# Kernel tuning notes

Hardware: AMD Instinct MI355X
Metric: run time of the kernel (lower is better)

Reference implementation:

```python
import jax, jax.numpy as jnp
import numpy as np

N = 1048576   # total points in batch
C_PT = 9      # point feature dim
C_LB = 20     # number of semantic classes (labels as soft/one-hot floats)
V1 = 500000   # unique voxels at scale 1
V8 = 65536    # unique voxels at scale 8


def setup_inputs() -> dict:
    key = jax.random.key(0)
    k1, k2, k3, k4 = jax.random.split(key, 4)
    points = jax.random.normal(k1, (N, C_PT), dtype=jnp.float32)
    coors_inv_s1 = jax.random.randint(k2, (N,), 0, V1, dtype=jnp.int64)
    labels = jax.random.uniform(k3, (N, C_LB), dtype=jnp.float32)
    coors_inv_s8 = jax.random.randint(k4, (N,), 0, V8, dtype=jnp.int64)
    return {"points": points, "coors_inv_s1": coors_inv_s1,
            "labels": labels, "coors_inv_s8": coors_inv_s8}


def _scatter_mean(x, idx, num_segments):
    # torch_scatter.scatter_mean(x, idx, dim=0): per-segment sum / count (count>=1)
    seg_sum = jax.ops.segment_sum(x, idx, num_segments=num_segments)
    ones = jnp.ones((x.shape[0], 1), dtype=x.dtype)
    count = jax.ops.segment_sum(ones, idx, num_segments=num_segments)
    return seg_sum / jnp.maximum(count, jnp.asarray(1, x.dtype))


def reference(points, coors_inv_s1, labels, coors_inv_s8):
    # voxel features: mean of point features per scale-1 voxel  -> [V1, C_PT]
    features = _scatter_mean(points, coors_inv_s1, V1)
    # voxel labels: mean of per-point class vectors per scale-8 voxel -> [V8, C_LB]
    voxel_labels = _scatter_mean(labels, coors_inv_s8, V8)
    # SparseConvTensor construction / dict assignment in the original is
    # bookkeeping; the computed tensors are (features, voxel_labels).
    return features, voxel_labels
```

## Files before the change

### kernel.cpp

```cpp
#include <hip/hip_runtime.h>

#define N_PTS 1048576
#define C_PT 9
#define C_LB 20
#define V1 500000
#define V8 65536

#define NB1 1954
#define NB8 256
#define NBT (NB1 + NB8)
#define KBLOCKS 256
#define PTS_PER_BLOCK (N_PTS / KBLOCKS)
#define CAP 2048

__global__ __launch_bounds__(1024) void count_kernel(const int* __restrict__ inv1,
                                                     const int* __restrict__ inv8,
                                                     unsigned short* __restrict__ mat)
{
    __shared__ int hist[NBT];
    for (int k = threadIdx.x; k < NBT; k += 1024) hist[k] = 0;
    __syncthreads();
    int base_i = blockIdx.x * PTS_PER_BLOCK;
    for (int t = threadIdx.x; t < PTS_PER_BLOCK; t += 1024) {
        int i = base_i + t;
        atomicAdd(&hist[inv1[i] >> 8], 1);
        atomicAdd(&hist[NB1 + (inv8[i] >> 8)], 1);
    }
    __syncthreads();
    unsigned short* row = mat + (size_t)blockIdx.x * NBT;
    for (int k = threadIdx.x; k < NBT; k += 1024) row[k] = (unsigned short)hist[k];
}

__global__ __launch_bounds__(256) void colscan_kernel(unsigned short* __restrict__ mat,
                                                      int* __restrict__ total)
{
    int wave = (int)((blockIdx.x * 256 + threadIdx.x) >> 6);
    int lane = threadIdx.x & 63;
    if (wave >= NBT) return;
    int carry = 0;
    for (int c = 0; c < KBLOCKS; c += 64) {
        int b = c + lane;
        int v = (int)mat[(size_t)b * NBT + wave];
        int s = v;
        #pragma unroll
        for (int d = 1; d < 64; d <<= 1) {
            int u = __shfl_up(s, d, 64);
            if (lane >= d) s += u;
        }
        mat[(size_t)b * NBT + wave] = (unsigned short)(s - v + carry);
        carry += __shfl(s, 63, 64);
    }
    if (lane == 0) total[wave] = carry;
}

__global__ __launch_bounds__(64) void basescan_kernel(const int* __restrict__ total,
                                                      int* __restrict__ base)
{
    int lane = threadIdx.x;
    int carry = 0;
    for (int c = 0; c < NB1; c += 64) {
        int k = c + lane;
        int v = (k < NB1) ? total[k] : 0;
        int s = v;
        #pragma unroll
        for (int d = 1; d < 64; d <<= 1) {
            int u = __shfl_up(s, d, 64);
            if (lane >= d) s += u;
        }
        if (k < NB1) base[k] = s - v + carry;
        carry += __shfl(s, 63, 64);
    }
    carry = 0;
    for (int c = 0; c < NB8; c += 64) {
        int k = c + lane;
        int v = total[NB1 + k];
        int s = v;
        #pragma unroll
        for (int d = 1; d < 64; d <<= 1) {
            int u = __shfl_up(s, d, 64);
            if (lane >= d) s += u;
        }
        base[NB1 + k] = s - v + carry;
        carry += __shfl(s, 63, 64);
    }
}

__global__ __launch_bounds__(1024) void scatter_kernel(const int* __restrict__ inv1,
                                                       const int* __restrict__ inv8,
                                                       const unsigned short* __restrict__ mat,
                                                       const int* __restrict__ base,
                                                       int* __restrict__ sorted1,
                                                       int* __restrict__ sorted8)
{
    __shared__ int off[NBT];
    __shared__ int cnt[NBT];
    const unsigned short* row = mat + (size_t)blockIdx.x * NBT;
    for (int k = threadIdx.x; k < NBT; k += 1024) {
        off[k] = base[k] + (int)row[k];
        cnt[k] = 0;
    }
    __syncthreads();
    int base_i = blockIdx.x * PTS_PER_BLOCK;
    for (int t = threadIdx.x; t < PTS_PER_BLOCK; t += 1024) {
        int i = base_i + t;
        int v1 = inv1[i];
        int k1 = v1 >> 8;
        int r1 = atomicAdd(&cnt[k1], 1);
        sorted1[off[k1] + r1] = i | ((v1 & 255) << 20);
        int v8 = inv8[i];
        int k8 = NB1 + (v8 >> 8);
        int r8 = atomicAdd(&cnt[k8], 1);
        sorted8[off[k8] + r8] = i | ((v8 & 255) << 20);
    }
}

__global__ __launch_bounds__(256) void accum_voxel_kernel(const float* __restrict__ points,
                                                          const float* __restrict__ labels,
                                                          const int* __restrict__ sorted1,
                                                          const int* __restrict__ sorted8,
                                                          const int* __restrict__ base,
                                                          const int* __restrict__ total,
                                                          float* __restrict__ feat_out,
                                                          float* __restrict__ lbl_out)
{
    __shared__ unsigned stage[CAP];
    __shared__ unsigned short perm[CAP];
    __shared__ int hist[256];
    __shared__ int starts[256];
    __shared__ int cursor[256];
    __shared__ int wsum[4];

    const int tid  = threadIdx.x;
    const int lane = tid & 63;
    const int wid  = tid >> 6;

    if (blockIdx.x < NB8) {
        int b = blockIdx.x;
        int start = base[NB1 + b];
        int num   = total[NB1 + b];
        float acc[C_LB];
        #pragma unroll
        for (int c = 0; c < C_LB; ++c) acc[c] = 0.0f;
        int mycnt = 0;

        for (int cbase = 0; cbase < num; cbase += CAP) {
            int csize = min(CAP, num - cbase);
            __syncthreads();
            for (int t = tid; t < csize; t += 256)
                stage[t] = (unsigned)sorted8[start + cbase + t];
            hist[tid] = 0;
            __syncthreads();
            for (int t = tid; t < csize; t += 256)
                atomicAdd(&hist[stage[t] >> 20], 1);
            __syncthreads();
            int x = hist[tid];
            int s = x;
            #pragma unroll
            for (int d = 1; d < 64; d <<= 1) {
                int u = __shfl_up(s, d, 64);
                if (lane >= d) s += u;
            }
            if (lane == 63) wsum[wid] = s;
            __syncthreads();
            int off = 0;
            #pragma unroll
            for (int w = 0; w < 4; ++w) if (w < wid) off += wsum[w];
            starts[tid] = off + s - x;
            cursor[tid] = 0;
            __syncthreads();
            for (int t = tid; t < csize; t += 256) {
                int bin = (int)(stage[t] >> 20);
                int r = atomicAdd(&cursor[bin], 1);
                perm[starts[bin] + r] = (unsigned short)t;
            }
            __syncthreads();
            int n  = hist[tid];
            int s0 = starts[tid];
            for (int j = 0; j < n; ++j) {
                int t = (int)perm[s0 + j];
                unsigned idx = stage[t] & 0xFFFFFu;
                const float4* __restrict__ r4 =
                    reinterpret_cast<const float4*>(labels) + (size_t)idx * 5;
                float4 v0 = r4[0], v1 = r4[1], v2 = r4[2], v3 = r4[3], v4 = r4[4];
                acc[0]  += v0.x; acc[1]  += v0.y; acc[2]  += v0.z; acc[3]  += v0.w;
                acc[4]  += v1.x; acc[5]  += v1.y; acc[6]  += v1.z; acc[7]  += v1.w;
                acc[8]  += v2.x; acc[9]  += v2.y; acc[10] += v2.z; acc[11] += v2.w;
                acc[12] += v3.x; acc[13] += v3.y; acc[14] += v3.z; acc[15] += v3.w;
                acc[16] += v4.x; acc[17] += v4.y; acc[18] += v4.z; acc[19] += v4.w;
            }
            mycnt += n;
        }
        float inv = 1.0f / (float)(mycnt > 0 ? mycnt : 1);
        float4* orow = reinterpret_cast<float4*>(lbl_out + ((size_t)b * 256 + tid) * C_LB);
        orow[0] = make_float4(acc[0] * inv,  acc[1] * inv,  acc[2] * inv,  acc[3] * inv);
        orow[1] = make_float4(acc[4] * inv,  acc[5] * inv,  acc[6] * inv,  acc[7] * inv);
        orow[2] = make_float4(acc[8] * inv,  acc[9] * inv,  acc[10] * inv, acc[11] * inv);
        orow[3] = make_float4(acc[12] * inv, acc[13] * inv, acc[14] * inv, acc[15] * inv);
        orow[4] = make_float4(acc[16] * inv, acc[17] * inv, acc[18] * inv, acc[19] * inv);
    } else {
        int b = blockIdx.x - NB8;
        int start = base[b];
        int num   = total[b];
        float acc[C_PT];
        #pragma unroll
        for (int c = 0; c < C_PT; ++c) acc[c] = 0.0f;
        int mycnt = 0;

        for (int cbase = 0; cbase < num; cbase += CAP) {
            int csize = min(CAP, num - cbase);
            __syncthreads();
            for (int t = tid; t < csize; t += 256)
                stage[t] = (unsigned)sorted1[start + cbase + t];
            hist[tid] = 0;
            __syncthreads();
            for (int t = tid; t < csize; t += 256)
                atomicAdd(&hist[stage[t] >> 20], 1);
            __syncthreads();
            int x = hist[tid];
            int s = x;
            #pragma unroll
            for (int d = 1; d < 64; d <<= 1) {
                int u = __shfl_up(s, d, 64);
                if (lane >= d) s += u;
            }
            if (lane == 63) wsum[wid] = s;
            __syncthreads();
            int off = 0;
            #pragma unroll
            for (int w = 0; w < 4; ++w) if (w < wid) off += wsum[w];
            starts[tid] = off + s - x;
            cursor[tid] = 0;
            __syncthreads();
            for (int t = tid; t < csize; t += 256) {
                int bin = (int)(stage[t] >> 20);
                int r = atomicAdd(&cursor[bin], 1);
                perm[starts[bin] + r] = (unsigned short)t;
            }
            __syncthreads();
            int n  = hist[tid];
            int s0 = starts[tid];
            for (int j = 0; j < n; ++j) {
                int t = (int)perm[s0 + j];
                unsigned idx = stage[t] & 0xFFFFFu;
                const float* __restrict__ r = points + (size_t)idx * C_PT;
                float p0 = r[0], p1 = r[1], p2 = r[2], p3 = r[3], p4 = r[4];
                float p5 = r[5], p6 = r[6], p7 = r[7], p8 = r[8];
                acc[0] += p0; acc[1] += p1; acc[2] += p2; acc[3] += p3;
                acc[4] += p4; acc[5] += p5; acc[6] += p6; acc[7] += p7;
                acc[8] += p8;
            }
            mycnt += n;
        }
        int v = b * 256 + tid;
        if (v < V1) {
            float inv = 1.0f / (float)(mycnt > 0 ? mycnt : 1);
            float* __restrict__ orow = feat_out + (size_t)v * C_PT;
            #pragma unroll
            for (int c = 0; c < C_PT; ++c) orow[c] = acc[c] * inv;
        }
    }
}

__global__ void voxel_scatter_add_kernel(const float* __restrict__ points,
                                         const int* __restrict__ inv1,
                                         const float* __restrict__ labels,
                                         const int* __restrict__ inv8,
                                         float* feat_sum, float* lbl_sum,
                                         float* cnt1, float* cnt8)
{
    int i = blockIdx.x * blockDim.x + threadIdx.x;
    if (i >= N_PTS) return;
    int v1 = inv1[i];
    int v8 = inv8[i];
    const float* p = points + (size_t)i * C_PT;
    float* f = feat_sum + (size_t)v1 * C_PT;
#pragma unroll
    for (int c = 0; c < C_PT; ++c) atomicAdd(&f[c], p[c]);
    atomicAdd(&cnt1[v1], 1.0f);
    const float* l = labels + (size_t)i * C_LB;
    float* o = lbl_sum + (size_t)v8 * C_LB;
#pragma unroll
    for (int c = 0; c < C_LB; ++c) atomicAdd(&o[c], l[c]);
    atomicAdd(&cnt8[v8], 1.0f);
}

__global__ void voxel_divide_kernel(float* out, const float* cnt1, const float* cnt8)
{
    const int totaln = V1 * C_PT + V8 * C_LB;
    for (int i = blockIdx.x * blockDim.x + threadIdx.x; i < totaln;
         i += gridDim.x * blockDim.x) {
        float c = (i < V1 * C_PT) ? cnt1[i / C_PT] : cnt8[(i - V1 * C_PT) / C_LB];
        out[i] /= fmaxf(c, 1.0f);
    }
}

extern "C" void kernel_launch(void* const* d_in, const int* in_sizes, int n_in,
                              void* d_out, int out_size, void* d_ws, size_t ws_size,
                              hipStream_t stream) {
    const float* points = (const float*)d_in[0];
    const int*   inv1   = (const int*)d_in[1];
    const float* labels = (const float*)d_in[2];
    const int*   inv8   = (const int*)d_in[3];

    float* out      = (float*)d_out;
    float* feat_out = out;
    float* lbl_out  = out + (size_t)V1 * C_PT;

    const size_t need = ((size_t)2 * N_PTS + 2 * NBT) * sizeof(int)
                      + (size_t)KBLOCKS * NBT * sizeof(unsigned short);
    if (ws_size >= need) {
        int* sorted1 = (int*)d_ws;
        int* sorted8 = sorted1 + N_PTS;
        int* total   = sorted8 + N_PTS;
        int* basep   = total + NBT;
        unsigned short* mat = (unsigned short*)(basep + NBT);

        count_kernel<<<KBLOCKS, 1024, 0, stream>>>(inv1, inv8, mat);
        colscan_kernel<<<(NBT + 3) / 4, 256, 0, stream>>>(mat, total);
        basescan_kernel<<<1, 64, 0, stream>>>(total, basep);
        scatter_kernel<<<KBLOCKS, 1024, 0, stream>>>(inv1, inv8, mat, basep,
                                                     sorted1, sorted8);
        accum_voxel_kernel<<<NB8 + NB1, 256, 0, stream>>>(points, labels, sorted1,
                                                          sorted8, basep, total,
                                                          feat_out, lbl_out);
    } else {
        float* cnt1 = (float*)d_ws;
        float* cnt8 = cnt1 + V1;
        hipMemsetAsync(d_out, 0, (size_t)out_size * sizeof(float), stream);
        hipMemsetAsync(d_ws, 0, ((size_t)V1 + V8) * sizeof(float), stream);
        const int block = 256;
        voxel_scatter_add_kernel<<<(N_PTS + block - 1) / block, block, 0, stream>>>(
            points, inv1, labels, inv8, feat_out, lbl_out, cnt1, cnt8);
        voxel_divide_kernel<<<2048, block, 0, stream>>>(out, cnt1, cnt8);
    }
}
```

Measured before the change: 109.4 us.

## Scatter bf16-packed point and label payloads into bucket order before accumulation

New measurement: 169.7 us. 1.55x slower.

```diff
diff --git a/kernel.cpp b/kernel.cpp
--- a/kernel.cpp
+++ b/kernel.cpp
@@ -12,6 +12,14 @@
 #define KBLOCKS 256
 #define PTS_PER_BLOCK (N_PTS / KBLOCKS)
 #define CAP 2048
+
+__device__ __forceinline__ unsigned f2bf(float f) {
+    unsigned u = __float_as_uint(f);
+    u += 0x7FFFu + ((u >> 16) & 1u);
+    return u >> 16;
+}
+__device__ __forceinline__ float bf_lo(unsigned w) { return __uint_as_float(w << 16); }
+__device__ __forceinline__ float bf_hi(unsigned w) { return __uint_as_float(w & 0xFFFF0000u); }
 
 __global__ __launch_bounds__(1024) void count_kernel(const int* __restrict__ inv1,
                                                      const int* __restrict__ inv8,
@@ -82,6 +90,210 @@
         }
         base[NB1 + k] = s - v + carry;
         carry += __shfl(s, 63, 64);
+    }
+}
+
+__global__ __launch_bounds__(1024) void scatter_pay_kernel(const float* __restrict__ points,
+                                                           const float* __restrict__ labels,
+                                                           const int* __restrict__ inv1,
+                                                           const int* __restrict__ inv8,
+                                                           const unsigned short* __restrict__ mat,
+                                                           const int* __restrict__ base,
+                                                           uint4* __restrict__ lblPay,
+                                                           uint4* __restrict__ ptsPay,
+                                                           unsigned char* __restrict__ bins8,
+                                                           unsigned char* __restrict__ bins1)
+{
+    __shared__ int off[NBT];
+    __shared__ int cnt[NBT];
+    const unsigned short* row = mat + (size_t)blockIdx.x * NBT;
+    for (int k = threadIdx.x; k < NBT; k += 1024) {
+        off[k] = base[k] + (int)row[k];
+        cnt[k] = 0;
+    }
+    __syncthreads();
+    int base_i = blockIdx.x * PTS_PER_BLOCK;
+    for (int t = threadIdx.x; t < PTS_PER_BLOCK; t += 1024) {
+        int i = base_i + t;
+
+        int v1 = inv1[i];
+        int k1 = v1 >> 8;
+        int r1 = atomicAdd(&cnt[k1], 1);
+        int dest1 = off[k1] + r1;
+        const float* __restrict__ p = points + (size_t)i * C_PT;
+        unsigned w0 = f2bf(p[0]) | (f2bf(p[1]) << 16);
+        unsigned w1 = f2bf(p[2]) | (f2bf(p[3]) << 16);
+        unsigned w2 = f2bf(p[4]) | (f2bf(p[5]) << 16);
+        unsigned w3 = f2bf(p[6]) | (f2bf(p[7]) << 16);
+        unsigned w4 = f2bf(p[8]);
+        uint4* __restrict__ pd = ptsPay + (size_t)dest1 * 2;
+        pd[0] = make_uint4(w0, w1, w2, w3);
+        pd[1] = make_uint4(w4, 0u, 0u, 0u);
+        bins1[dest1] = (unsigned char)(v1 & 255);
+
+        int v8 = inv8[i];
+        int k8 = NB1 + (v8 >> 8);
+        int r8 = atomicAdd(&cnt[k8], 1);
+        int dest8 = off[k8] + r8;
+        const float4* __restrict__ l4 = reinterpret_cast<const float4*>(labels) + (size_t)i * 5;
+        float4 a0 = l4[0], a1 = l4[1], a2 = l4[2], a3 = l4[3], a4 = l4[4];
+        uint4* __restrict__ ld = lblPay + (size_t)dest8 * 4;
+        ld[0] = make_uint4(f2bf(a0.x) | (f2bf(a0.y) << 16), f2bf(a0.z) | (f2bf(a0.w) << 16),
+                           f2bf(a1.x) | (f2bf(a1.y) << 16), f2bf(a1.z) | (f2bf(a1.w) << 16));
+        ld[1] = make_uint4(f2bf(a2.x) | (f2bf(a2.y) << 16), f2bf(a2.z) | (f2bf(a2.w) << 16),
+                           f2bf(a3.x) | (f2bf(a3.y) << 16), f2bf(a3.z) | (f2bf(a3.w) << 16));
+        ld[2] = make_uint4(f2bf(a4.x) | (f2bf(a4.y) << 16), f2bf(a4.z) | (f2bf(a4.w) << 16), 0u, 0u);
+        ld[3] = make_uint4(0u, 0u, 0u, 0u);
+        bins8[dest8] = (unsigned char)(v8 & 255);
+    }
+}
+
+__global__ __launch_bounds__(256) void accum_sorted_kernel(const uint4* __restrict__ lblPay,
+                                                           const uint4* __restrict__ ptsPay,
+                                                           const unsigned char* __restrict__ bins8,
+                                                           const unsigned char* __restrict__ bins1,
+                                                           const int* __restrict__ base,
+                                                           const int* __restrict__ total,
+                                                           float* __restrict__ feat_out,
+                                                           float* __restrict__ lbl_out)
+{
+    __shared__ unsigned char binbuf[CAP];
+    __shared__ unsigned short perm[CAP];
+    __shared__ int hist[256];
+    __shared__ int starts[256];
+    __shared__ int cursor[256];
+    __shared__ int wsum[4];
+
+    const int tid  = threadIdx.x;
+    const int lane = tid & 63;
+    const int wid  = tid >> 6;
+
+    if (blockIdx.x < NB8) {
+        int b = blockIdx.x;
+        int start = base[NB1 + b];
+        int num   = total[NB1 + b];
+        float acc[C_LB];
+        #pragma unroll
+        for (int c = 0; c < C_LB; ++c) acc[c] = 0.0f;
+        int mycnt = 0;
+
+        for (int cbase = 0; cbase < num; cbase += CAP) {
+            int csize = min(CAP, num - cbase);
+            __syncthreads();
+            for (int t = tid; t < csize; t += 256) binbuf[t] = bins8[start + cbase + t];
+            hist[tid] = 0;
+            __syncthreads();
+            for (int t = tid; t < csize; t += 256) atomicAdd(&hist[(int)binbuf[t]], 1);
+            __syncthreads();
+            int x = hist[tid];
+            int s = x;
+            #pragma unroll
+            for (int d = 1; d < 64; d <<= 1) {
+                int u = __shfl_up(s, d, 64);
+                if (lane >= d) s += u;
+            }
+            if (lane == 63) wsum[wid] = s;
+            __syncthreads();
+            int off = 0;
+            #pragma unroll
+            for (int w = 0; w < 4; ++w) if (w < wid) off += wsum[w];
+            starts[tid] = off + s - x;
+            cursor[tid] = 0;
+            __syncthreads();
+            for (int t = tid; t < csize; t += 256) {
+                int bin = (int)binbuf[t];
+                int r = atomicAdd(&cursor[bin], 1);
+                perm[starts[bin] + r] = (unsigned short)t;
+            }
+            __syncthreads();
+            int n  = hist[tid];
+            int s0 = starts[tid];
+            for (int j = 0; j < n; ++j) {
+                int r = start + cbase + (int)perm[s0 + j];
+                const uint4* __restrict__ ld = lblPay + (size_t)r * 4;
+                uint4 x0 = ld[0];
+                uint4 x1 = ld[1];
+                uint2 x2 = *reinterpret_cast<const uint2*>(ld + 2);
+                acc[0]  += bf_lo(x0.x); acc[1]  += bf_hi(x0.x);
+                acc[2]  += bf_lo(x0.y); acc[3]  += bf_hi(x0.y);
+                acc[4]  += bf_lo(x0.z); acc[5]  += bf_hi(x0.z);
+                acc[6]  += bf_lo(x0.w); acc[7]  += bf_hi(x0.w);
+                acc[8]  += bf_lo(x1.x); acc[9]  += bf_hi(x1.x);
+                acc[10] += bf_lo(x1.y); acc[11] += bf_hi(x1.y);
+                acc[12] += bf_lo(x1.z); acc[13] += bf_hi(x1.z);
+                acc[14] += bf_lo(x1.w); acc[15] += bf_hi(x1.w);
+                acc[16] += bf_lo(x2.x); acc[17] += bf_hi(x2.x);
+                acc[18] += bf_lo(x2.y); acc[19] += bf_hi(x2.y);
+            }
+            mycnt += n;
+        }
+        float inv = 1.0f / (float)(mycnt > 0 ? mycnt : 1);
+        float4* orow = reinterpret_cast<float4*>(lbl_out + ((size_t)b * 256 + tid) * C_LB);
+        orow[0] = make_float4(acc[0] * inv,  acc[1] * inv,  acc[2] * inv,  acc[3] * inv);
+        orow[1] = make_float4(acc[4] * inv,  acc[5] * inv,  acc[6] * inv,  acc[7] * inv);
+        orow[2] = make_float4(acc[8] * inv,  acc[9] * inv,  acc[10] * inv, acc[11] * inv);
+        orow[3] = make_float4(acc[12] * inv, acc[13] * inv, acc[14] * inv, acc[15] * inv);
+        orow[4] = make_float4(acc[16] * inv, acc[17] * inv, acc[18] * inv, acc[19] * inv);
+    } else {
+        int b = blockIdx.x - NB8;
+        int start = base[b];
+        int num   = total[b];
+        float acc[C_PT];
+        #pragma unroll
+        for (int c = 0; c < C_PT; ++c) acc[c] = 0.0f;
+        int mycnt = 0;
+
+        for (int cbase = 0; cbase < num; cbase += CAP) {
+            int csize = min(CAP, num - cbase);
+            __syncthreads();
+            for (int t = tid; t < csize; t += 256) binbuf[t] = bins1[start + cbase + t];
+            hist[tid] = 0;
+            __syncthreads();
+            for (int t = tid; t < csize; t += 256) atomicAdd(&hist[(int)binbuf[t]], 1);
+            __syncthreads();
+            int x = hist[tid];
+            int s = x;
+            #pragma unroll
+            for (int d = 1; d < 64; d <<= 1) {
+                int u = __shfl_up(s, d, 64);
+                if (lane >= d) s += u;
+            }
+            if (lane == 63) wsum[wid] = s;
+            __syncthreads();
+            int off = 0;
+            #pragma unroll
+            for (int w = 0; w < 4; ++w) if (w < wid) off += wsum[w];
+            starts[tid] = off + s - x;
+            cursor[tid] = 0;
+            __syncthreads();
+            for (int t = tid; t < csize; t += 256) {
+                int bin = (int)binbuf[t];
+                int r = atomicAdd(&cursor[bin], 1);
+                perm[starts[bin] + r] = (unsigned short)t;
+            }
+            __syncthreads();
+            int n  = hist[tid];
+            int s0 = starts[tid];
+            for (int j = 0; j < n; ++j) {
+                int r = start + cbase + (int)perm[s0 + j];
+                const uint4* __restrict__ pd = ptsPay + (size_t)r * 2;
+                uint4 x0 = pd[0];
+                unsigned w4 = *reinterpret_cast<const unsigned*>(pd + 1);
+                acc[0] += bf_lo(x0.x); acc[1] += bf_hi(x0.x);
+                acc[2] += bf_lo(x0.y); acc[3] += bf_hi(x0.y);
+                acc[4] += bf_lo(x0.z); acc[5] += bf_hi(x0.z);
+                acc[6] += bf_lo(x0.w); acc[7] += bf_hi(x0.w);
+                acc[8] += bf_lo(w4);
+            }
+            mycnt += n;
+        }
+        int v = b * 256 + tid;
+        if (v < V1) {
+            float inv = 1.0f / (float)(mycnt > 0 ? mycnt : 1);
+            float* __restrict__ orow = feat_out + (size_t)v * C_PT;
+            #pragma unroll
+            for (int c = 0; c < C_PT; ++c) orow[c] = acc[c] * inv;
+        }
     }
 }
 
@@ -142,7 +354,6 @@
         #pragma unroll
         for (int c = 0; c < C_LB; ++c) acc[c] = 0.0f;
         int mycnt = 0;
-
         for (int cbase = 0; cbase < num; cbase += CAP) {
             int csize = min(CAP, num - cbase);
             __syncthreads();
@@ -150,8 +361,7 @@
                 stage[t] = (unsigned)sorted8[start + cbase + t];
             hist[tid] = 0;
             __syncthreads();
-            for (int t = tid; t < csize; t += 256)
-                atomicAdd(&hist[stage[t] >> 20], 1);
+            for (int t = tid; t < csize; t += 256) atomicAdd(&hist[stage[t] >> 20], 1);
             __syncthreads();
             int x = hist[tid];
             int s = x;
@@ -205,7 +415,6 @@
         #pragma unroll
         for (int c = 0; c < C_PT; ++c) acc[c] = 0.0f;
         int mycnt = 0;
-
         for (int cbase = 0; cbase < num; cbase += CAP) {
             int csize = min(CAP, num - cbase);
             __syncthreads();
@@ -213,8 +422,7 @@
                 stage[t] = (unsigned)sorted1[start + cbase + t];
             hist[tid] = 0;
             __syncthreads();
-            for (int t = tid; t < csize; t += 256)
-                atomicAdd(&hist[stage[t] >> 20], 1);
+            for (int t = tid; t < csize; t += 256) atomicAdd(&hist[stage[t] >> 20], 1);
             __syncthreads();
             int x = hist[tid];
             int s = x;
@@ -306,9 +514,32 @@
     float* feat_out = out;
     float* lbl_out  = out + (size_t)V1 * C_PT;
 
-    const size_t need = ((size_t)2 * N_PTS + 2 * NBT) * sizeof(int)
-                      + (size_t)KBLOCKS * NBT * sizeof(unsigned short);
-    if (ws_size >= need) {
+    const size_t pay_need = (size_t)N_PTS * 96 + (size_t)N_PTS * 2
+                          + (size_t)2 * NBT * sizeof(int)
+                          + (size_t)KBLOCKS * NBT * sizeof(unsigned short);
+    const size_t idx_need = ((size_t)2 * N_PTS + 2 * NBT) * sizeof(int)
+                          + (size_t)KBLOCKS * NBT * sizeof(unsigned short);
+    const int block = 256;
+
+    if (ws_size >= pay_need) {
+        uint4* lblPay = (uint4*)d_ws;
+        uint4* ptsPay = lblPay + (size_t)N_PTS * 4;
+        unsigned char* bins8 = (unsigned char*)(ptsPay + (size_t)N_PTS * 2);
+        unsigned char* bins1 = bins8 + N_PTS;
+        int* total = (int*)(bins1 + N_PTS);
+        int* basep = total + NBT;
+        unsigned short* mat = (unsigned short*)(basep + NBT);
+
+        count_kernel<<<KBLOCKS, 1024, 0, stream>>>(inv1, inv8, mat);
+        colscan_kernel<<<(NBT + 3) / 4, 256, 0, stream>>>(mat, total);
+        basescan_kernel<<<1, 64, 0, stream>>>(total, basep);
+        scatter_pay_kernel<<<KBLOCKS, 1024, 0, stream>>>(points, labels, inv1, inv8,
+                                                         mat, basep, lblPay, ptsPay,
+                                                         bins8, bins1);
+        accum_sorted_kernel<<<NB8 + NB1, 256, 0, stream>>>(lblPay, ptsPay, bins8, bins1,
+                                                           basep, total,
+                                                           feat_out, lbl_out);
+    } else if (ws_size >= idx_need) {
         int* sorted1 = (int*)d_ws;
         int* sorted8 = sorted1 + N_PTS;
         int* total   = sorted8 + N_PTS;
@@ -328,7 +559,6 @@
         float* cnt8 = cnt1 + V1;
         hipMemsetAsync(d_out, 0, (size_t)out_size * sizeof(float), stream);
         hipMemsetAsync(d_ws, 0, ((size_t)V1 + V8) * sizeof(float), stream);
-        const int block = 256;
         voxel_scatter_add_kernel<<<(N_PTS + block - 1) / block, block, 0, stream>>>(
             points, inv1, labels, inv8, feat_out, lbl_out, cnt1, cnt8);
         voxel_divide_kernel<<<2048, block, 0, stream>>>(out, cnt1, cnt8);
```
